# Optimization experiments

Hardware: AMD Instinct MI355X
Metric: run time of the kernel (lower is better)

Reference implementation:

```python
import jax, jax.numpy as jnp
import numpy as np

N_NODES = 100000
NEG_SLOPE = 0.2


def leaky_relu(x):
    return jnp.where(x >= 0, x, NEG_SLOPE * x)


def gat_conv(x, src, dst, W, a_src, a_dst, b, heads, out_ch, concat):
    # x: [N, F_in]; src/dst: [E]; W: [F_in, heads*out_ch]
    n = x.shape[0]
    h = (x @ W).reshape(n, heads, out_ch)                      # [N, H, C]
    s_src = jnp.einsum('nhc,hc->nh', h, a_src)                 # [N, H]
    s_dst = jnp.einsum('nhc,hc->nh', h, a_dst)                 # [N, H]
    e = leaky_relu(s_src[src] + s_dst[dst])                    # [E, H]
    # segment softmax over incoming edges of each dst node
    m = jax.ops.segment_max(e, dst, num_segments=n)            # [N, H]
    m = jnp.where(jnp.isfinite(m), m, 0.0)
    p = jnp.exp(e - m[dst])                                    # [E, H]
    denom = jax.ops.segment_sum(p, dst, num_segments=n)        # [N, H]
    alpha = p / denom[dst]                                     # [E, H]
    out = jax.ops.segment_sum(h[src] * alpha[..., None], dst, num_segments=n)  # [N, H, C]
    if concat:
        out = out.reshape(n, heads * out_ch)
    else:
        out = out.mean(axis=1)
    return out + b


def setup_inputs() -> dict:
    key = jax.random.key(0)
    ks = jax.random.split(key, 10)
    F_in, hidden, heads, n_cls = 128, 32, 8, 40
    n_edges = 1600000
    x = jax.random.normal(ks[0], (N_NODES, F_in), dtype=jnp.float32)
    edge_index = jax.random.randint(ks[1], (2, n_edges), 0, N_NODES, dtype=jnp.int64)
    s = 0.1
    W1 = jax.random.normal(ks[2], (F_in, heads * hidden), dtype=jnp.float32) * s
    att_src1 = jax.random.normal(ks[3], (heads, hidden), dtype=jnp.float32) * s
    att_dst1 = jax.random.normal(ks[4], (heads, hidden), dtype=jnp.float32) * s
    b1 = jnp.zeros((heads * hidden,), dtype=jnp.float32)
    W2 = jax.random.normal(ks[5], (heads * hidden, n_cls), dtype=jnp.float32) * s
    att_src2 = jax.random.normal(ks[6], (1, n_cls), dtype=jnp.float32) * s
    att_dst2 = jax.random.normal(ks[7], (1, n_cls), dtype=jnp.float32) * s
    b2 = jnp.zeros((n_cls,), dtype=jnp.float32)
    return {
        'x': x, 'edge_index': edge_index,
        'W1': W1, 'att_src1': att_src1, 'att_dst1': att_dst1, 'b1': b1,
        'W2': W2, 'att_src2': att_src2, 'att_dst2': att_dst2, 'b2': b2,
    }


def reference(x, edge_index, W1, att_src1, att_dst1, b1, W2, att_src2, att_dst2, b2):
    n = x.shape[0]
    # PyG GATConv default: add self loops
    loop = jnp.arange(n, dtype=edge_index.dtype)
    src = jnp.concatenate([edge_index[0], loop])
    dst = jnp.concatenate([edge_index[1], loop])
    h = gat_conv(x, src, dst, W1, att_src1, att_dst1, b1, heads=8, out_ch=32, concat=True)
    h = jax.nn.relu(h)  # dropout p=0 / eval mode: identity
    out = gat_conv(h, src, dst, W2, att_src2, att_dst2, b2, heads=1, out_ch=40, concat=True)
    return jax.nn.log_softmax(out, axis=1)
```

## Files before the change

kernel.cpp:

```cpp
#include <hip/hip_runtime.h>
#include <hip/hip_bf16.h>
#include <cmath>


typedef unsigned short ushortT;
typedef unsigned int uintT;
typedef unsigned char ucharT;
typedef __attribute__((ext_vector_type(8))) short short8;
typedef __attribute__((ext_vector_type(4))) float float4v;
typedef __attribute__((ext_vector_type(2))) float float2v;

static __device__ __forceinline__ float bflo(uintT u) {
    return __uint_as_float(u << 16);
}
static __device__ __forceinline__ float bfhi(uintT u) {
    return __uint_as_float(u & 0xffff0000u);
}
static __device__ __forceinline__ ushortT f2bf(float f) {
    __hip_bfloat16 h = __float2bfloat16(f);
    return *reinterpret_cast<ushortT*>(&h);
}
static __device__ __forceinline__ uintT pk(float a, float b) {
    return (uintT)f2bf(a) | ((uintT)f2bf(b) << 16);
}
static __device__ __forceinline__ float ub(uintT u, int k) {
    return (float)((u >> (8 * k)) & 0xffu);
}
static __device__ __forceinline__ float lrelu(float e) {
    return 0.6f * e + 0.4f * fabsf(e);
}

#define PREP_BLOCKS 184
#define EPB 4096

__global__ __launch_bounds__(256) void k_prep(const float* __restrict__ W1,
                                              const float* __restrict__ W2,
                                              const float* __restrict__ a1s,
                                              const float* __restrict__ a1d,
                                              ushortT* __restrict__ W1t,
                                              ushortT* __restrict__ W2t) {
    int t = blockIdx.x * 256 + threadIdx.x;
    if (t < 128 * 256) {
        int k = t >> 8, s = t & 255;
        int c = ((s & 15) << 4) | (s >> 4);
        W1t[s * 128 + k] = f2bf(W1[(size_t)k * 256 + c]);
    } else if (t < 128 * 256 + 48 * 256) {
        int q = t - 128 * 256;
        int k = q / 48, c = q - k * 48;
        W2t[c * 256 + k] = (c < 40) ? f2bf(W2[k * 40 + c]) : (ushortT)0;
    } else if (t < 128 * 256 + 48 * 256 + 2048) {
        int q = t - (128 * 256 + 48 * 256);
        int k = q >> 4, j = q & 15;
        int h = j & 7;
        const float* av = ((j < 8) ? a1s : a1d) + h * 32;
        const float* wr = W1 + (size_t)k * 256 + h * 32;
        float s = 0.f;
        #pragma unroll
        for (int c = 0; c < 32; ++c) s += wr[c] * av[c];
        W1t[(256 + j) * 128 + k] = f2bf(s);
    }
}

static __device__ __forceinline__ void dev_gemm1(int slab,
                                                 const float* __restrict__ A,
                                                 const ushortT* __restrict__ Bt,
                                                 ucharT* __restrict__ h1i,
                                                 float* __restrict__ hsc,
                                                 float* __restrict__ s1s,
                                                 float* __restrict__ s1d, int M) {
    int lane = threadIdx.x & 63;
    int r0 = slab * 16;
    if (r0 >= M) return;
    int n = lane & 15, q = lane >> 4;
    const float* arow = A + (size_t)(r0 + n) * 128 + q * 8;
    short8 af[4];
    #pragma unroll
    for (int s = 0; s < 4; ++s) {
        float4 v0 = *(const float4*)(arow + s * 32);
        float4 v1 = *(const float4*)(arow + s * 32 + 4);
        short8 a;
        a[0] = (short)f2bf(v0.x); a[1] = (short)f2bf(v0.y);
        a[2] = (short)f2bf(v0.z); a[3] = (short)f2bf(v0.w);
        a[4] = (short)f2bf(v1.x); a[5] = (short)f2bf(v1.y);
        a[6] = (short)f2bf(v1.z); a[7] = (short)f2bf(v1.w);
        af[s] = a;
    }
    float4v acc[17];
    #pragma unroll
    for (int j = 0; j < 17; ++j) acc[j] = (float4v){0.f, 0.f, 0.f, 0.f};
    #pragma unroll
    for (int s = 0; s < 4; ++s) {
        #pragma unroll
        for (int j = 0; j < 17; ++j) {
            short8 b = *(const short8*)(Bt + (size_t)(j * 16 + n) * 128 + s * 32 + q * 8);
            acc[j] = __builtin_amdgcn_mfma_f32_16x16x32_bf16(af[s], b, acc[j], 0, 0, 0);
        }
    }
    float am[4];
    #pragma unroll
    for (int r = 0; r < 4; ++r) {
        float m = 0.f;
        #pragma unroll
        for (int j = 0; j < 16; ++j) m = fmaxf(m, fabsf(acc[j][r]));
        am[r] = m;
    }
    #pragma unroll
    for (int off = 1; off < 16; off <<= 1) {
        #pragma unroll
        for (int r = 0; r < 4; ++r) am[r] = fmaxf(am[r], __shfl_xor(am[r], off, 64));
    }
    #pragma unroll
    for (int r = 0; r < 4; ++r) {
        int row = r0 + q * 4 + r;
        float m = am[r];
        float si = (m > 0.f) ? 127.f / m : 0.f;
        uintT wd[4];
        #pragma unroll
        for (int wq = 0; wq < 4; ++wq) {
            uintT p4 = 0;
            #pragma unroll
            for (int b = 0; b < 4; ++b) {
                int j = wq * 4 + b;
                int qv = (int)rintf(acc[j][r] * si) + 128;
                p4 |= ((uintT)(qv & 0xff)) << (8 * b);
            }
            wd[wq] = p4;
        }
        uint4 o = make_uint4(wd[0], wd[1], wd[2], wd[3]);
        *(uint4*)(h1i + (size_t)row * 256 + n * 16) = o;
        if (n == 0) hsc[row] = m * (1.f / 127.f);
        float vv = acc[16][r];
        if (n < 8) s1s[(size_t)row * 8 + n] = vv;
        else       s1d[(size_t)row * 8 + (n - 8)] = vv;
    }
}

__global__ __launch_bounds__(256) void k_cnt_g1(const int* __restrict__ ei, int E,
                                                int* __restrict__ counts, int nbuck,
                                                const float* __restrict__ A,
                                                const ushortT* __restrict__ Bt,
                                                ucharT* __restrict__ h1i,
                                                float* __restrict__ hsc,
                                                float* __restrict__ s1s,
                                                float* __restrict__ s1d,
                                                int M, int nPrim, int slabBase) {
    if (blockIdx.x >= nPrim) {
        int wave = threadIdx.x >> 6;
        int slab = slabBase + (blockIdx.x - nPrim) * 4 + wave;
        dev_gemm1(slab, A, Bt, h1i, hsc, s1s, s1d, M);
        return;
    }
    __shared__ int h[1024];
    int t = threadIdx.x;
    for (int i = t; i < nbuck; i += 256) h[i] = 0;
    __syncthreads();
    int base = blockIdx.x * EPB;
    #pragma unroll
    for (int r = 0; r < 4; ++r) {
        int i4 = base + (r * 256 + t) * 4;
        if (i4 + 3 < E) {
            int4 d = *(const int4*)(ei + E + i4);
            atomicAdd(&h[d.x >> 7], 1);
            atomicAdd(&h[d.y >> 7], 1);
            atomicAdd(&h[d.z >> 7], 1);
            atomicAdd(&h[d.w >> 7], 1);
        } else {
            for (int j = i4; j < E; ++j) atomicAdd(&h[ei[E + j] >> 7], 1);
        }
    }
    __syncthreads();
    int* crow = counts + (size_t)blockIdx.x * nbuck;
    for (int i = t; i < nbuck; i += 256) crow[i] = h[i];
}

__global__ __launch_bounds__(256) void k_scan_cols(int* __restrict__ counts,
                                                   int* __restrict__ totals,
                                                   int nb1, int nbuck) {
    __shared__ int wsum[4];
    int k = blockIdx.x;
    int t = threadIdx.x, lane = t & 63, wv = t >> 6;
    int e0 = 2 * t, e1 = 2 * t + 1;
    int v0 = (e0 < nb1) ? counts[(size_t)e0 * nbuck + k] : 0;
    int v1 = (e1 < nb1) ? counts[(size_t)e1 * nbuck + k] : 0;
    int s = v0 + v1;
    int incl = s;
    #pragma unroll
    for (int off = 1; off < 64; off <<= 1) {
        int u = __shfl_up(incl, off, 64);
        if (lane >= off) incl += u;
    }
    if (lane == 63) wsum[wv] = incl;
    __syncthreads();
    int add = 0;
    if (wv > 0) add += wsum[0];
    if (wv > 1) add += wsum[1];
    if (wv > 2) add += wsum[2];
    incl += add;
    int excl = incl - s;
    if (e0 < nb1) counts[(size_t)e0 * nbuck + k] = excl;
    if (e1 < nb1) counts[(size_t)e1 * nbuck + k] = excl + v0;
    if (t == 255) totals[k] = incl;
}

__global__ __launch_bounds__(256) void k_place_g1(const int* __restrict__ ei, int E,
                                                  const int* __restrict__ counts,
                                                  const int* __restrict__ totals,
                                                  int* __restrict__ bstart,
                                                  uintT* __restrict__ tmp, int nbuck,
                                                  const float* __restrict__ A,
                                                  const ushortT* __restrict__ Bt,
                                                  ucharT* __restrict__ h1i,
                                                  float* __restrict__ hsc,
                                                  float* __restrict__ s1s,
                                                  float* __restrict__ s1d,
                                                  int M, int nPrim, int slabBase) {
    if (blockIdx.x >= nPrim) {
        int wave = threadIdx.x >> 6;
        int slab = slabBase + (blockIdx.x - nPrim) * 4 + wave;
        dev_gemm1(slab, A, Bt, h1i, hsc, s1s, s1d, M);
        return;
    }
    __shared__ int st[1024];
    __shared__ int pos[1024];
    __shared__ int wsum[4];
    int t = threadIdx.x, lane = t & 63, wv = t >> 6;
    int b = blockIdx.x;
    int g[4];
    int s = 0;
    #pragma unroll
    for (int j = 0; j < 4; ++j) {
        int e = 4 * t + j;
        g[j] = (e < nbuck) ? totals[e] : 0;
        s += g[j];
    }
    int incl = s;
    #pragma unroll
    for (int off = 1; off < 64; off <<= 1) {
        int u = __shfl_up(incl, off, 64);
        if (lane >= off) incl += u;
    }
    if (lane == 63) wsum[wv] = incl;
    __syncthreads();
    int add = 0;
    if (wv > 0) add += wsum[0];
    if (wv > 1) add += wsum[1];
    if (wv > 2) add += wsum[2];
    int excl = incl + add - s;
    #pragma unroll
    for (int j = 0; j < 4; ++j) {
        int e = 4 * t + j;
        if (e < nbuck) st[e] = excl;
        excl += g[j];
    }
    __syncthreads();
    const int* crow = counts + (size_t)b * nbuck;
    for (int i = t; i < nbuck; i += 256) {
        int sv = st[i];
        pos[i] = sv + crow[i];
        if (b == 0) bstart[i] = sv;
    }
    __syncthreads();
    int base = b * EPB;
    #pragma unroll
    for (int r = 0; r < 4; ++r) {
        int i4 = base + (r * 256 + t) * 4;
        if (i4 + 3 < E) {
            int4 sv = *(const int4*)(ei + i4);
            int4 dv = *(const int4*)(ei + E + i4);
            int p0 = atomicAdd(&pos[dv.x >> 7], 1);
            tmp[p0] = (uintT)sv.x | (((uintT)dv.x & 127u) << 17);
            int p1 = atomicAdd(&pos[dv.y >> 7], 1);
            tmp[p1] = (uintT)sv.y | (((uintT)dv.y & 127u) << 17);
            int p2 = atomicAdd(&pos[dv.z >> 7], 1);
            tmp[p2] = (uintT)sv.z | (((uintT)dv.z & 127u) << 17);
            int p3 = atomicAdd(&pos[dv.w >> 7], 1);
            tmp[p3] = (uintT)sv.w | (((uintT)dv.w & 127u) << 17);
        } else {
            for (int j = i4; j < E; ++j) {
                int sj = ei[j], dj = ei[E + j];
                int p = atomicAdd(&pos[dj >> 7], 1);
                tmp[p] = (uintT)sj | (((uintT)dj & 127u) << 17);
            }
        }
    }
}

__global__ __launch_bounds__(256) void k_csr_g1(const uintT* __restrict__ tmp,
                                                const int* __restrict__ bstart,
                                                const int* __restrict__ totals,
                                                int* __restrict__ rowptr,
                                                int* __restrict__ csr_src,
                                                int N, int nbuck,
                                                const float* __restrict__ A,
                                                const ushortT* __restrict__ Bt,
                                                ucharT* __restrict__ h1i,
                                                float* __restrict__ hsc,
                                                float* __restrict__ s1s,
                                                float* __restrict__ s1d,
                                                int M, int nPrim, int slabBase) {
    if (blockIdx.x >= nPrim) {
        int wave = threadIdx.x >> 6;
        int slab = slabBase + (blockIdx.x - nPrim) * 4 + wave;
        dev_gemm1(slab, A, Bt, h1i, hsc, s1s, s1d, M);
        return;
    }
    __shared__ int cnt[128];
    __shared__ int cur[128];
    __shared__ int wtot;
    int k = blockIdx.x;
    int t = threadIdx.x;
    int nodeBase = k << 7;
    int nn = N - nodeBase;
    if (nn > 128) nn = 128;
    int myStart = bstart[k];
    int myCount = totals[k];
    int csrBase = myStart + nodeBase;
    if (t < 128) cnt[t] = 0;
    __syncthreads();
    for (int i = t; i < myCount; i += 256) {
        uintT p = tmp[myStart + i];
        atomicAdd(&cnt[p >> 17], 1);
    }
    __syncthreads();
    int dseg = 0, incl = 0;
    if (t < 128) {
        dseg = (t < nn) ? cnt[t] + 1 : 0;
        incl = dseg;
        #pragma unroll
        for (int off = 1; off < 64; off <<= 1) {
            int u = __shfl_up(incl, off, 64);
            if ((t & 63) >= off) incl += u;
        }
        if (t == 63) wtot = incl;
    }
    __syncthreads();
    if (t < nn) {
        int excl = incl - dseg + ((t >= 64) ? wtot : 0);
        int rp = csrBase + excl;
        int node = nodeBase + t;
        rowptr[node + 1] = rp + dseg;
        csr_src[rp] = node;
        cur[t] = rp + 1;
    }
    if (k == 0 && t == 0) rowptr[0] = 0;
    __syncthreads();
    for (int i = t; i < myCount; i += 256) {
        uintT p = tmp[myStart + i];
        int ld = p >> 17;
        int q = atomicAdd(&cur[ld], 1);
        csr_src[q] = (int)(p & 0x1FFFFu);
    }
}

struct Edge1 {
    float sv, sc;
    uint4 v;
};

static __device__ __forceinline__ void ld1(Edge1& S, int j, int end,
                                           const int* __restrict__ csr_src,
                                           const float* __restrict__ ssrc,
                                           const float* __restrict__ hsc,
                                           const ucharT* __restrict__ hb, int head) {
    if (j < end) {
        int s = csr_src[j];
        S.sv = ssrc[(size_t)s * 8 + head];
        S.sc = hsc[s];
        S.v = *(const uint4*)(hb + (size_t)s * 256);
    }
}

static __device__ __forceinline__ void ac1(const Edge1& S, float sdn,
                                           float2v* A, float& l, float& sps) {
    float p = __expf(lrelu(S.sv + sdn));
    l += p;
    float ps = p * S.sc;
    sps += ps;
    float2v p2 = {ps, ps};
    uintT w;
    w = S.v.x;
    A[0] += p2 * (float2v){ub(w, 0), ub(w, 1)};
    A[1] += p2 * (float2v){ub(w, 2), ub(w, 3)};
    w = S.v.y;
    A[2] += p2 * (float2v){ub(w, 0), ub(w, 1)};
    A[3] += p2 * (float2v){ub(w, 2), ub(w, 3)};
    w = S.v.z;
    A[4] += p2 * (float2v){ub(w, 0), ub(w, 1)};
    A[5] += p2 * (float2v){ub(w, 2), ub(w, 3)};
    w = S.v.w;
    A[6] += p2 * (float2v){ub(w, 0), ub(w, 1)};
    A[7] += p2 * (float2v){ub(w, 2), ub(w, 3)};
}

__global__ __launch_bounds__(256) void k_agg1(const ucharT* __restrict__ h1i,
                                              const float* __restrict__ hsc,
                                              const float* __restrict__ ssrc,
                                              const float* __restrict__ sdst,
                                              const int* __restrict__ rowptr,
                                              const int* __restrict__ csr_src,
                                              const float* __restrict__ b1,
                                              ushortT* __restrict__ out1, int N) {
    int lane = threadIdx.x & 63;
    int wid = threadIdx.x >> 6;
    int n = blockIdx.x * 4 + wid;
    if (n >= N) return;
    int g = lane >> 4;
    int cl = lane & 15;
    int head = cl >> 1;
    int beg = rowptr[n], end = rowptr[n + 1];
    float sdn = sdst[(size_t)n * 8 + head];
    const ucharT* hb = h1i + cl * 16;
    float2v A[8];
    #pragma unroll
    for (int k = 0; k < 8; ++k) A[k] = (float2v){0.f, 0.f};
    float l = 0.f, sps = 0.f;
    int i0 = beg + g;
    if (i0 < end) {
        Edge1 S0, S1, S2;
        S0.sv = S1.sv = S2.sv = 0.f;
        S0.sc = S1.sc = S2.sc = 0.f;
        S0.v = S1.v = S2.v = make_uint4(0u, 0u, 0u, 0u);
        ld1(S0, i0, end, csr_src, ssrc, hsc, hb, head);
        ld1(S1, i0 + 4, end, csr_src, ssrc, hsc, hb, head);
        ld1(S2, i0 + 8, end, csr_src, ssrc, hsc, hb, head);
        for (int idx = i0; idx < end; idx += 12) {
            ac1(S0, sdn, A, l, sps);
            ld1(S0, idx + 12, end, csr_src, ssrc, hsc, hb, head);
            if (idx + 4 < end) {
                ac1(S1, sdn, A, l, sps);
                ld1(S1, idx + 16, end, csr_src, ssrc, hsc, hb, head);
            }
            if (idx + 8 < end) {
                ac1(S2, sdn, A, l, sps);
                ld1(S2, idx + 20, end, csr_src, ssrc, hsc, hb, head);
            }
        }
    }
    #pragma unroll
    for (int off = 16; off < 64; off <<= 1) {
        l += __shfl_xor(l, off, 64);
        sps += __shfl_xor(sps, off, 64);
        #pragma unroll
        for (int k = 0; k < 8; ++k) {
            A[k].x += __shfl_xor(A[k].x, off, 64);
            A[k].y += __shfl_xor(A[k].y, off, 64);
        }
    }
    if (g == 0) {
        float inv = 1.f / l;
        float adj = 128.f * sps;
        const float4 bb0 = *(const float4*)(b1 + cl * 16);
        const float4 bb1 = *(const float4*)(b1 + cl * 16 + 4);
        const float4 bb2 = *(const float4*)(b1 + cl * 16 + 8);
        const float4 bb3 = *(const float4*)(b1 + cl * 16 + 12);
        float bbf[16] = {bb0.x, bb0.y, bb0.z, bb0.w, bb1.x, bb1.y, bb1.z, bb1.w,
                         bb2.x, bb2.y, bb2.z, bb2.w, bb3.x, bb3.y, bb3.z, bb3.w};
        uintT o[8];
        #pragma unroll
        for (int k = 0; k < 8; ++k) {
            float x0 = fmaxf((A[k].x - adj) * inv + bbf[2 * k], 0.f);
            float x1 = fmaxf((A[k].y - adj) * inv + bbf[2 * k + 1], 0.f);
            o[k] = pk(x0, x1);
        }
        *(uint4*)(out1 + (size_t)n * 256 + cl * 16) =
            make_uint4(o[0], o[1], o[2], o[3]);
        *(uint4*)(out1 + (size_t)n * 256 + cl * 16 + 8) =
            make_uint4(o[4], o[5], o[6], o[7]);
    }
}

__global__ __launch_bounds__(256) void k_gemm2(const ushortT* __restrict__ X,
                                               const ushortT* __restrict__ Bt,
                                               const float* __restrict__ a2s,
                                               const float* __restrict__ a2d,
                                               ushortT* __restrict__ H2,
                                               float* __restrict__ s2s,
                                               float* __restrict__ s2d, int M) {
    int lane = threadIdx.x & 63, wave = threadIdx.x >> 6;
    int slab = blockIdx.x * 4 + wave;
    int r0 = slab * 16;
    if (r0 >= M) return;
    int n = lane & 15, q = lane >> 4;
    const ushortT* xrow = X + (size_t)(r0 + n) * 256 + q * 8;
    float4v acc[3];
    #pragma unroll
    for (int j = 0; j < 3; ++j) acc[j] = (float4v){0.f, 0.f, 0.f, 0.f};
    #pragma unroll
    for (int s = 0; s < 8; ++s) {
        short8 a = *(const short8*)(xrow + s * 32);
        #pragma unroll
        for (int j = 0; j < 3; ++j) {
            short8 b = *(const short8*)(Bt + (size_t)(j * 16 + n) * 256 + s * 32 + q * 8);
            acc[j] = __builtin_amdgcn_mfma_f32_16x16x32_bf16(a, b, acc[j], 0, 0, 0);
        }
    }
    float asv[3], adv[3];
    #pragma unroll
    for (int j = 0; j < 3; ++j) {
        int col = j * 16 + n;
        asv[j] = (col < 40) ? a2s[col] : 0.f;
        adv[j] = (col < 40) ? a2d[col] : 0.f;
    }
    float us[4], ud[4];
    #pragma unroll
    for (int r = 0; r < 4; ++r) {
        us[r] = acc[0][r] * asv[0] + acc[1][r] * asv[1] + acc[2][r] * asv[2];
        ud[r] = acc[0][r] * adv[0] + acc[1][r] * adv[1] + acc[2][r] * adv[2];
    }
    #pragma unroll
    for (int off = 1; off < 16; off <<= 1) {
        #pragma unroll
        for (int r = 0; r < 4; ++r) {
            us[r] += __shfl_xor(us[r], off, 64);
            ud[r] += __shfl_xor(ud[r], off, 64);
        }
    }
    #pragma unroll
    for (int j = 0; j < 3; ++j) {
        int col = j * 16 + n;
        if (col < 40) {
            #pragma unroll
            for (int r = 0; r < 4; ++r)
                H2[(size_t)(r0 + q * 4 + r) * 40 + col] = f2bf(acc[j][r]);
        }
    }
    if (n == 0) {
        #pragma unroll
        for (int r = 0; r < 4; ++r) {
            int row = r0 + q * 4 + r;
            s2s[row] = us[r];
            s2d[row] = ud[r];
        }
    }
}

struct Edge2 {
    float sv;
    uint2 v;
};

static __device__ __forceinline__ void ld2(Edge2& S, int j, int end,
                                           const int* __restrict__ csr_src,
                                           const float* __restrict__ ss,
                                           const ushortT* __restrict__ h2, int cl) {
    if (j < end) {
        int s = csr_src[j];
        S.sv = ss[s];
        S.v = *(const uint2*)(h2 + (size_t)s * 40 + cl * 4);
    }
}

static __device__ __forceinline__ void ac2(const Edge2& S, float sdn,
                                           float2v& A01, float2v& A23, float& l) {
    float p = __expf(lrelu(S.sv + sdn));
    l += p;
    float2v p2 = {p, p};
    A01 += p2 * (float2v){bflo(S.v.x), bfhi(S.v.x)};
    A23 += p2 * (float2v){bflo(S.v.y), bfhi(S.v.y)};
}

__global__ __launch_bounds__(256) void k_agg2lsm(const ushortT* __restrict__ h2,
                                                 const float* __restrict__ ss,
                                                 const float* __restrict__ sd,
                                                 const int* __restrict__ rowptr,
                                                 const int* __restrict__ csr_src,
                                                 const float* __restrict__ b2,
                                                 float* __restrict__ out, int N) {
    int lane = threadIdx.x & 63;
    int wid = threadIdx.x >> 6;
    int n = blockIdx.x * 4 + wid;
    if (n >= N) return;
    int el = lane / 10;
    int cl = lane - el * 10;
    int beg = rowptr[n], end = rowptr[n + 1];
    float sdn = sd[n];
    float2v A01 = (float2v){0.f, 0.f}, A23 = (float2v){0.f, 0.f};
    float l = 0.f;
    if (el < 6) {
        int i0 = beg + el;
        if (i0 < end) {
            Edge2 S0, S1, S2;
            S0.sv = S1.sv = S2.sv = 0.f;
            S0.v = S1.v = S2.v = make_uint2(0u, 0u);
            ld2(S0, i0, end, csr_src, ss, h2, cl);
            ld2(S1, i0 + 6, end, csr_src, ss, h2, cl);
            ld2(S2, i0 + 12, end, csr_src, ss, h2, cl);
            for (int idx = i0; idx < end; idx += 18) {
                ac2(S0, sdn, A01, A23, l);
                ld2(S0, idx + 18, end, csr_src, ss, h2, cl);
                if (idx + 6 < end) {
                    ac2(S1, sdn, A01, A23, l);
                    ld2(S1, idx + 24, end, csr_src, ss, h2, cl);
                }
                if (idx + 12 < end) {
                    ac2(S2, sdn, A01, A23, l);
                    ld2(S2, idx + 30, end, csr_src, ss, h2, cl);
                }
            }
        }
    }
    float a0 = A01.x, a1 = A01.y, a2 = A23.x, a3 = A23.y;
    float t0 = 0.f, t1 = 0.f, t2 = 0.f, t3 = 0.f, lt = 0.f;
    #pragma unroll
    for (int k = 0; k < 6; ++k) {
        int sl = cl + 10 * k;
        t0 += __shfl(a0, sl, 64);
        t1 += __shfl(a1, sl, 64);
        t2 += __shfl(a2, sl, 64);
        t3 += __shfl(a3, sl, 64);
        if (cl == 0) lt += __shfl(l, sl, 64);
    }
    lt = __shfl(lt, 0, 64);
    float inv = 1.f / lt;
    float o0 = t0 * inv + b2[cl * 4 + 0];
    float o1 = t1 * inv + b2[cl * 4 + 1];
    float o2 = t2 * inv + b2[cl * 4 + 2];
    float o3 = t3 * inv + b2[cl * 4 + 3];
    float lm = (lane < 10) ? fmaxf(fmaxf(o0, o1), fmaxf(o2, o3)) : -INFINITY;
    #pragma unroll
    for (int off = 32; off; off >>= 1) lm = fmaxf(lm, __shfl_xor(lm, off, 64));
    float le = (lane < 10)
        ? __expf(o0 - lm) + __expf(o1 - lm) + __expf(o2 - lm) + __expf(o3 - lm)
        : 0.f;
    #pragma unroll
    for (int off = 32; off; off >>= 1) le += __shfl_xor(le, off, 64);
    float ls = lm + logf(le);
    if (lane < 10) {
        float4 w = make_float4(o0 - ls, o1 - ls, o2 - ls, o3 - ls);
        *(float4*)(out + (size_t)n * 40 + cl * 4) = w;
    }
}

extern "C" void kernel_launch(void* const* d_in, const int* in_sizes, int n_in,
                              void* d_out, int out_size, void* d_ws, size_t ws_size,
                              hipStream_t stream) {
    const float* x   = (const float*)d_in[0];
    const int*   ei  = (const int*)d_in[1];
    const float* W1  = (const float*)d_in[2];
    const float* a1s = (const float*)d_in[3];
    const float* a1d = (const float*)d_in[4];
    const float* b1  = (const float*)d_in[5];
    const float* W2  = (const float*)d_in[6];
    const float* a2s = (const float*)d_in[7];
    const float* a2d = (const float*)d_in[8];
    const float* b2  = (const float*)d_in[9];
    float* out = (float*)d_out;

    const int N = in_sizes[0] / 128;
    const int E = in_sizes[1] / 2;
    const int ET = E + N;
    const int NBUCK = (N + 127) >> 7;
    const int NB1 = (E + EPB - 1) / EPB;

    char* w = (char*)d_ws;
    ucharT* h1i = (ucharT*)w;
    float* hsc  = (float*)(w + (size_t)N * 256);
    ushortT* out1b = (ushortT*)(w + (size_t)N * 256 + (size_t)N * 4);
    float* s1s  = (float*)(out1b + (size_t)N * 256);
    float* s1d  = s1s + (size_t)N * 8;
    int* i_cnt = (int*)(s1d + (size_t)N * 8);
    int* i_tot = i_cnt + (size_t)NB1 * NBUCK;
    int* i_bst = i_tot + NBUCK + 2;
    int* i_row = i_bst + NBUCK + 2;
    uintT* i_tmp = (uintT*)(i_row + N + 16);
    int* i_csr = (int*)(i_tmp + E);
    ushortT* W1t = (ushortT*)(i_csr + ET);
    ushortT* W2t = W1t + 272 * 128;
    ushortT* h2b = (ushortT*)w;
    float* s2s = (float*)(w + (size_t)N * 40 * 2);
    float* s2d = s2s + N;

    const int nb4 = (N + 3) / 4;
    const int nbG = (N / 16 + 3) / 4;
    const int CH  = (nbG + 2) / 3;

    k_prep<<<PREP_BLOCKS, 256, 0, stream>>>(W1, W2, a1s, a1d, W1t, W2t);
    k_cnt_g1<<<NB1 + CH, 256, 0, stream>>>(ei, E, i_cnt, NBUCK,
                                           x, W1t, h1i, hsc, s1s, s1d,
                                           N, NB1, 0);
    k_scan_cols<<<NBUCK, 256, 0, stream>>>(i_cnt, i_tot, NB1, NBUCK);
    k_place_g1<<<NB1 + CH, 256, 0, stream>>>(ei, E, i_cnt, i_tot, i_bst, i_tmp, NBUCK,
                                             x, W1t, h1i, hsc, s1s, s1d,
                                             N, NB1, CH * 4);
    k_csr_g1<<<NBUCK + CH, 256, 0, stream>>>(i_tmp, i_bst, i_tot, i_row, i_csr,
                                             N, NBUCK,
                                             x, W1t, h1i, hsc, s1s, s1d,
                                             N, NBUCK, CH * 8);

    k_agg1<<<nb4, 256, 0, stream>>>(h1i, hsc, s1s, s1d, i_row, i_csr, b1, out1b, N);

    k_gemm2<<<nbG, 256, 0, stream>>>(out1b, W2t, a2s, a2d, h2b, s2s, s2d, N);
    k_agg2lsm<<<nb4, 256, 0, stream>>>(h2b, s2s, s2d, i_row, i_csr, b2, out, N);
}
```

Measured before the change: 398.0 us.

## Pack per-source scores with features and prefetch CSR indices further ahead

Layer 1 now stores each source node's per-head attention score and its quantization scale together in one 9-float record, so every edge gather touches one contiguous region. Layer 2 does the same by keeping the source score in the padding of a 48-element feature row. Both aggregation loops split the index load from the value loads and fetch CSR indices a full pipeline stage ahead, using a clamped index so the loads stay in bounds. The workspace is rearranged to hold the new buffers, including an aliasing of s2d into the tmp region, which risks overlap bugs if the sizes assumed there do not hold.

```diff
diff --git a/kernel.cpp b/kernel.cpp
--- a/kernel.cpp
+++ b/kernel.cpp
@@ -65,8 +65,7 @@
                                                  const float* __restrict__ A,
                                                  const ushortT* __restrict__ Bt,
                                                  ucharT* __restrict__ h1i,
-                                                 float* __restrict__ hsc,
-                                                 float* __restrict__ s1s,
+                                                 float* __restrict__ s1c,
                                                  float* __restrict__ s1d, int M) {
     int lane = threadIdx.x & 63;
     int r0 = slab * 16;
@@ -128,9 +127,9 @@
         }
         uint4 o = make_uint4(wd[0], wd[1], wd[2], wd[3]);
         *(uint4*)(h1i + (size_t)row * 256 + n * 16) = o;
-        if (n == 0) hsc[row] = m * (1.f / 127.f);
+        if (n == 0) s1c[(size_t)row * 9 + 8] = m * (1.f / 127.f);
         float vv = acc[16][r];
-        if (n < 8) s1s[(size_t)row * 8 + n] = vv;
+        if (n < 8) s1c[(size_t)row * 9 + n] = vv;
         else       s1d[(size_t)row * 8 + (n - 8)] = vv;
     }
 }
@@ -140,14 +139,13 @@
                                                 const float* __restrict__ A,
                                                 const ushortT* __restrict__ Bt,
                                                 ucharT* __restrict__ h1i,
-                                                float* __restrict__ hsc,
-                                                float* __restrict__ s1s,
+                                                float* __restrict__ s1c,
                                                 float* __restrict__ s1d,
                                                 int M, int nPrim, int slabBase) {
     if (blockIdx.x >= nPrim) {
         int wave = threadIdx.x >> 6;
         int slab = slabBase + (blockIdx.x - nPrim) * 4 + wave;
-        dev_gemm1(slab, A, Bt, h1i, hsc, s1s, s1d, M);
+        dev_gemm1(slab, A, Bt, h1i, s1c, s1d, M);
         return;
     }
     __shared__ int h[1024];
@@ -210,14 +208,13 @@
                                                   const float* __restrict__ A,
                                                   const ushortT* __restrict__ Bt,
                                                   ucharT* __restrict__ h1i,
-                                                  float* __restrict__ hsc,
-                                                  float* __restrict__ s1s,
+                                                  float* __restrict__ s1c,
                                                   float* __restrict__ s1d,
                                                   int M, int nPrim, int slabBase) {
     if (blockIdx.x >= nPrim) {
         int wave = threadIdx.x >> 6;
         int slab = slabBase + (blockIdx.x - nPrim) * 4 + wave;
-        dev_gemm1(slab, A, Bt, h1i, hsc, s1s, s1d, M);
+        dev_gemm1(slab, A, Bt, h1i, s1c, s1d, M);
         return;
     }
     __shared__ int st[1024];
@@ -294,14 +291,13 @@
                                                 const float* __restrict__ A,
                                                 const ushortT* __restrict__ Bt,
                                                 ucharT* __restrict__ h1i,
-                                                float* __restrict__ hsc,
-                                                float* __restrict__ s1s,
+                                                float* __restrict__ s1c,
                                                 float* __restrict__ s1d,
                                                 int M, int nPrim, int slabBase) {
     if (blockIdx.x >= nPrim) {
         int wave = threadIdx.x >> 6;
         int slab = slabBase + (blockIdx.x - nPrim) * 4 + wave;
-        dev_gemm1(slab, A, Bt, h1i, hsc, s1s, s1d, M);
+        dev_gemm1(slab, A, Bt, h1i, s1c, s1d, M);
         return;
     }
     __shared__ int cnt[128];
@@ -355,17 +351,23 @@
 struct Edge1 {
     float sv, sc;
     uint4 v;
+    int si;
 };
 
-static __device__ __forceinline__ void ld1(Edge1& S, int j, int end,
-                                           const int* __restrict__ csr_src,
-                                           const float* __restrict__ ssrc,
-                                           const float* __restrict__ hsc,
-                                           const ucharT* __restrict__ hb, int head) {
+static __device__ __forceinline__ void ldi1(Edge1& S, int j, int endm1,
+                                            const int* __restrict__ csr_src) {
+    int jj = j < endm1 ? j : endm1;
+    S.si = csr_src[jj];
+}
+
+static __device__ __forceinline__ void ldv1(Edge1& S, int j, int end,
+                                            const float* __restrict__ s1c,
+                                            const ucharT* __restrict__ hb, int head) {
     if (j < end) {
-        int s = csr_src[j];
-        S.sv = ssrc[(size_t)s * 8 + head];
-        S.sc = hsc[s];
+        int s = S.si;
+        const float* sb = s1c + (size_t)s * 9;
+        S.sv = sb[head];
+        S.sc = sb[8];
         S.v = *(const uint4*)(hb + (size_t)s * 256);
     }
 }
@@ -393,9 +395,8 @@
 }
 
 __global__ __launch_bounds__(256) void k_agg1(const ucharT* __restrict__ h1i,
-                                              const float* __restrict__ hsc,
-                                              const float* __restrict__ ssrc,
-                                              const float* __restrict__ sdst,
+                                              const float* __restrict__ s1c,
+                                              const float* __restrict__ s1d,
                                               const int* __restrict__ rowptr,
                                               const int* __restrict__ csr_src,
                                               const float* __restrict__ b1,
@@ -408,7 +409,7 @@
     int cl = lane & 15;
     int head = cl >> 1;
     int beg = rowptr[n], end = rowptr[n + 1];
-    float sdn = sdst[(size_t)n * 8 + head];
+    float sdn = s1d[(size_t)n * 8 + head];
     const ucharT* hb = h1i + cl * 16;
     float2v A[8];
     #pragma unroll
@@ -416,23 +417,33 @@
     float l = 0.f, sps = 0.f;
     int i0 = beg + g;
     if (i0 < end) {
+        int endm1 = end - 1;
         Edge1 S0, S1, S2;
         S0.sv = S1.sv = S2.sv = 0.f;
         S0.sc = S1.sc = S2.sc = 0.f;
         S0.v = S1.v = S2.v = make_uint4(0u, 0u, 0u, 0u);
-        ld1(S0, i0, end, csr_src, ssrc, hsc, hb, head);
-        ld1(S1, i0 + 4, end, csr_src, ssrc, hsc, hb, head);
-        ld1(S2, i0 + 8, end, csr_src, ssrc, hsc, hb, head);
+        ldi1(S0, i0, endm1, csr_src);
+        ldi1(S1, i0 + 4, endm1, csr_src);
+        ldi1(S2, i0 + 8, endm1, csr_src);
+        ldv1(S0, i0, end, s1c, hb, head);
+        ldv1(S1, i0 + 4, end, s1c, hb, head);
+        ldv1(S2, i0 + 8, end, s1c, hb, head);
+        ldi1(S0, i0 + 12, endm1, csr_src);
+        ldi1(S1, i0 + 16, endm1, csr_src);
+        ldi1(S2, i0 + 20, endm1, csr_src);
         for (int idx = i0; idx < end; idx += 12) {
             ac1(S0, sdn, A, l, sps);
-            ld1(S0, idx + 12, end, csr_src, ssrc, hsc, hb, head);
+            ldv1(S0, idx + 12, end, s1c, hb, head);
+            ldi1(S0, idx + 24, endm1, csr_src);
             if (idx + 4 < end) {
                 ac1(S1, sdn, A, l, sps);
-                ld1(S1, idx + 16, end, csr_src, ssrc, hsc, hb, head);
+                ldv1(S1, idx + 16, end, s1c, hb, head);
+                ldi1(S1, idx + 28, endm1, csr_src);
             }
             if (idx + 8 < end) {
                 ac1(S2, sdn, A, l, sps);
-                ld1(S2, idx + 20, end, csr_src, ssrc, hsc, hb, head);
+                ldv1(S2, idx + 20, end, s1c, hb, head);
+                ldi1(S2, idx + 32, endm1, csr_src);
             }
         }
     }
@@ -474,7 +485,6 @@
                                                const float* __restrict__ a2s,
                                                const float* __restrict__ a2d,
                                                ushortT* __restrict__ H2,
-                                               float* __restrict__ s2s,
                                                float* __restrict__ s2d, int M) {
     int lane = threadIdx.x & 63, wave = threadIdx.x >> 6;
     int slab = blockIdx.x * 4 + wave;
@@ -521,14 +531,14 @@
         if (col < 40) {
             #pragma unroll
             for (int r = 0; r < 4; ++r)
-                H2[(size_t)(r0 + q * 4 + r) * 40 + col] = f2bf(acc[j][r]);
+                H2[(size_t)(r0 + q * 4 + r) * 48 + col] = f2bf(acc[j][r]);
         }
     }
     if (n == 0) {
         #pragma unroll
         for (int r = 0; r < 4; ++r) {
             int row = r0 + q * 4 + r;
-            s2s[row] = us[r];
+            *(float*)(H2 + (size_t)row * 48 + 40) = us[r];
             s2d[row] = ud[r];
         }
     }
@@ -537,16 +547,22 @@
 struct Edge2 {
     float sv;
     uint2 v;
+    int si;
 };
 
-static __device__ __forceinline__ void ld2(Edge2& S, int j, int end,
-                                           const int* __restrict__ csr_src,
-                                           const float* __restrict__ ss,
-                                           const ushortT* __restrict__ h2, int cl) {
+static __device__ __forceinline__ void ldi2(Edge2& S, int j, int endm1,
+                                            const int* __restrict__ csr_src) {
+    int jj = j < endm1 ? j : endm1;
+    S.si = csr_src[jj];
+}
+
+static __device__ __forceinline__ void ldv2(Edge2& S, int j, int end,
+                                            const ushortT* __restrict__ h2, int cl) {
     if (j < end) {
-        int s = csr_src[j];
-        S.sv = ss[s];
-        S.v = *(const uint2*)(h2 + (size_t)s * 40 + cl * 4);
+        int s = S.si;
+        const ushortT* hr = h2 + (size_t)s * 48;
+        S.v = *(const uint2*)(hr + cl * 4);
+        S.sv = *(const float*)(hr + 40);
     }
 }
 
@@ -560,7 +576,6 @@
 }
 
 __global__ __launch_bounds__(256) void k_agg2lsm(const ushortT* __restrict__ h2,
-                                                 const float* __restrict__ ss,
                                                  const float* __restrict__ sd,
                                                  const int* __restrict__ rowptr,
                                                  const int* __restrict__ csr_src,
@@ -579,22 +594,32 @@
     if (el < 6) {
         int i0 = beg + el;
         if (i0 < end) {
+            int endm1 = end - 1;
             Edge2 S0, S1, S2;
             S0.sv = S1.sv = S2.sv = 0.f;
             S0.v = S1.v = S2.v = make_uint2(0u, 0u);
-            ld2(S0, i0, end, csr_src, ss, h2, cl);
-            ld2(S1, i0 + 6, end, csr_src, ss, h2, cl);
-            ld2(S2, i0 + 12, end, csr_src, ss, h2, cl);
+            ldi2(S0, i0, endm1, csr_src);
+            ldi2(S1, i0 + 6, endm1, csr_src);
+            ldi2(S2, i0 + 12, endm1, csr_src);
+            ldv2(S0, i0, end, h2, cl);
+            ldv2(S1, i0 + 6, end, h2, cl);
+            ldv2(S2, i0 + 12, end, h2, cl);
+            ldi2(S0, i0 + 18, endm1, csr_src);
+            ldi2(S1, i0 + 24, endm1, csr_src);
+            ldi2(S2, i0 + 30, endm1, csr_src);
             for (int idx = i0; idx < end; idx += 18) {
                 ac2(S0, sdn, A01, A23, l);
-                ld2(S0, idx + 18, end, csr_src, ss, h2, cl);
+                ldv2(S0, idx + 18, end, h2, cl);
+                ldi2(S0, idx + 36, endm1, csr_src);
                 if (idx + 6 < end) {
                     ac2(S1, sdn, A01, A23, l);
-                    ld2(S1, idx + 24, end, csr_src, ss, h2, cl);
+                    ldv2(S1, idx + 24, end, h2, cl);
+                    ldi2(S1, idx + 42, endm1, csr_src);
                 }
                 if (idx + 12 < end) {
                     ac2(S2, sdn, A01, A23, l);
-                    ld2(S2, idx + 30, end, csr_src, ss, h2, cl);
+                    ldv2(S2, idx + 30, end, h2, cl);
+                    ldi2(S2, idx + 48, endm1, csr_src);
                 }
             }
         }
@@ -654,21 +679,19 @@
 
     char* w = (char*)d_ws;
     ucharT* h1i = (ucharT*)w;
-    float* hsc  = (float*)(w + (size_t)N * 256);
-    ushortT* out1b = (ushortT*)(w + (size_t)N * 256 + (size_t)N * 4);
-    float* s1s  = (float*)(out1b + (size_t)N * 256);
-    float* s1d  = s1s + (size_t)N * 8;
+    ushortT* out1b = (ushortT*)(w + (size_t)N * 256);
+    int* i_row = (int*)(w + (size_t)N * 768);
+    float* s1c = (float*)(w + (size_t)N * 768 + ((size_t)N + 16) * 4);
+    float* s1d = s1c + (size_t)N * 9;
     int* i_cnt = (int*)(s1d + (size_t)N * 8);
     int* i_tot = i_cnt + (size_t)NB1 * NBUCK;
     int* i_bst = i_tot + NBUCK + 2;
-    int* i_row = i_bst + NBUCK + 2;
-    uintT* i_tmp = (uintT*)(i_row + N + 16);
+    uintT* i_tmp = (uintT*)(i_bst + NBUCK + 2);
     int* i_csr = (int*)(i_tmp + E);
     ushortT* W1t = (ushortT*)(i_csr + ET);
     ushortT* W2t = W1t + 272 * 128;
-    ushortT* h2b = (ushortT*)w;
-    float* s2s = (float*)(w + (size_t)N * 40 * 2);
-    float* s2d = s2s + N;
+    ushortT* h2b = (ushortT*)s1c;
+    float* s2d = (float*)(i_tmp + (size_t)(E - N - 16));
 
     const int nb4 = (N + 3) / 4;
     const int nbG = (N / 16 + 3) / 4;
@@ -676,19 +699,19 @@
 
     k_prep<<<PREP_BLOCKS, 256, 0, stream>>>(W1, W2, a1s, a1d, W1t, W2t);
     k_cnt_g1<<<NB1 + CH, 256, 0, stream>>>(ei, E, i_cnt, NBUCK,
-                                           x, W1t, h1i, hsc, s1s, s1d,
+                                           x, W1t, h1i, s1c, s1d,
                                            N, NB1, 0);
     k_scan_cols<<<NBUCK, 256, 0, stream>>>(i_cnt, i_tot, NB1, NBUCK);
     k_place_g1<<<NB1 + CH, 256, 0, stream>>>(ei, E, i_cnt, i_tot, i_bst, i_tmp, NBUCK,
-                                             x, W1t, h1i, hsc, s1s, s1d,
+                                             x, W1t, h1i, s1c, s1d,
                                              N, NB1, CH * 4);
     k_csr_g1<<<NBUCK + CH, 256, 0, stream>>>(i_tmp, i_bst, i_tot, i_row, i_csr,
                                              N, NBUCK,
-                                             x, W1t, h1i, hsc, s1s, s1d,
+                                             x, W1t, h1i, s1c, s1d,
                                              N, NBUCK, CH * 8);
 
-    k_agg1<<<nb4, 256, 0, stream>>>(h1i, hsc, s1s, s1d, i_row, i_csr, b1, out1b, N);
-
-    k_gemm2<<<nbG, 256, 0, stream>>>(out1b, W2t, a2s, a2d, h2b, s2s, s2d, N);
-    k_agg2lsm<<<nb4, 256, 0, stream>>>(h2b, s2s, s2d, i_row, i_csr, b2, out, N);
-}
+    k_agg1<<<nb4, 256, 0, stream>>>(h1i, s1c, s1d, i_row, i_csr, b1, out1b, N);
+
+    k_gemm2<<<nbG, 256, 0, stream>>>(out1b, W2t, a2s, a2d, h2b, s2d, N);
+    k_agg2lsm<<<nb4, 256, 0, stream>>>(h2b, s2d, i_row, i_csr, b2, out, N);
+}
```

New measurement: 400.1 us. Within noise of the previous version (+0.5%).
